# Kernel optimization log

Hardware: AMD Instinct MI355X
Metric: run time of the kernel (lower is better)

The kernel has to match this reference:

```python
import jax, jax.numpy as jnp
import numpy as np

DIM_IN = 10000
LW = [512, 512]
EW = [16, 16]


def setup_inputs() -> dict:
    key = jax.random.key(0)
    ks = jax.random.split(key, 16)
    x = jax.random.normal(ks[0], (4096, DIM_IN), dtype=jnp.float32)
    mask = jax.random.randint(ks[1], (4096, DIM_IN), 0, 2).astype(jnp.float32)
    s = 0.02
    # LNet: dim_in -> 512 -> 512 -> dim_in (tanh after hidden layers only)
    W1 = jax.random.normal(ks[2], (DIM_IN, LW[0]), dtype=jnp.float32) * s
    b1 = jnp.zeros((LW[0],), jnp.float32)
    W2 = jax.random.normal(ks[3], (LW[0], LW[1]), dtype=jnp.float32) * s
    b2 = jnp.zeros((LW[1],), jnp.float32)
    W3 = jax.random.normal(ks[4], (LW[1], DIM_IN), dtype=jnp.float32) * s
    b3 = jnp.zeros((DIM_IN,), jnp.float32)
    # ENet: 1 -> 16 -> 16 -> 1
    E1w = jax.random.normal(ks[5], (1, EW[0]), dtype=jnp.float32) * s
    E1b = jnp.zeros((EW[0],), jnp.float32)
    E2w = jax.random.normal(ks[6], (EW[0], EW[1]), dtype=jnp.float32) * s
    E2b = jnp.zeros((EW[1],), jnp.float32)
    E3w = jax.random.normal(ks[7], (EW[1], 1), dtype=jnp.float32) * s
    E3b = jnp.zeros((1,), jnp.float32)
    return {"x": x, "mask": mask, "W1": W1, "b1": b1, "W2": W2, "b2": b2,
            "W3": W3, "b3": b3, "E1w": E1w, "E1b": E1b, "E2w": E2w,
            "E2b": E2b, "E3w": E3w, "E3b": E3b}


def reference(x, mask, W1, b1, W2, b2, W3, b3, E1w, E1b, E2w, E2b, E3w, E3b):
    # LNet: two tanh hidden layers + final linear
    h = jnp.tanh(x @ W1 + b1)            # [B, 512]
    h = jnp.tanh(h @ W2 + b2)            # [B, 512]
    out = h @ W3 + b3                    # [B, dim_in]
    # ENet applied elementwise to scalar entries; original gathers x[mask>0],
    # runs ENet, adds 0.8*y residual, scatters back. Equivalent dense form:
    v = out[..., None]                   # [B, dim_in, 1]
    e = jnp.tanh(v @ E1w + E1b)          # [B, dim_in, 16]
    e = jnp.tanh(e @ E2w + E2b)          # [B, dim_in, 16]
    e = (e @ E3w + E3b)[..., 0]          # [B, dim_in]
    y = e + 0.8 * out
    return jnp.where(mask > 0, y, out)
```

## Files before the change

kernel.cpp:

```cpp
#include <hip/hip_runtime.h>
#include <stdint.h>

typedef unsigned short u16;
typedef u16 u16x8 __attribute__((ext_vector_type(8)));
typedef __bf16 bf16x8 __attribute__((ext_vector_type(8)));
typedef float f32x4 __attribute__((ext_vector_type(4)));

__device__ __forceinline__ float b2f(u16 u) {
    union { unsigned int i; float f; } c; c.i = ((unsigned int)u) << 16; return c.f;
}
__device__ __forceinline__ u16 f2b(float f) {
    unsigned int u = __float_as_uint(f);
    u += 0x7fff + ((u >> 16) & 1);
    return (u16)(u >> 16);
}

typedef const __attribute__((address_space(1))) unsigned int* gas_p;
typedef __attribute__((address_space(3))) unsigned int* las_p;
__device__ __forceinline__ void gll16(const void* g, void* l) {
    __builtin_amdgcn_global_load_lds((gas_p)g, (las_p)l, 16, 0, 0);
}

__global__ __launch_bounds__(1024) void detect_dtype(const u16* __restrict__ m,
                                                     int* __restrict__ flag) {
    __shared__ int s;
    int t = threadIdx.x;
    if (t == 0) s = 0;
    __syncthreads();
    if (m[2 * t] != 0) atomicOr(&s, 1);
    __syncthreads();
    if (t == 0) *flag = s;
}

__global__ __launch_bounds__(256) void canon_params(
        const void* b1, const void* b2, const void* b3,
        const void* E1w, const void* E1b, const void* E2w,
        const void* E2b, const void* E3w, const void* E3b,
        const int* __restrict__ flag, float* __restrict__ dst) {
    const int DT = *flag;
    int i = blockIdx.x * 256 + threadIdx.x;
    if (i >= 11345) return;
    const void* srcs[9] = {b1, b2, b3, E1w, E1b, E2w, E2b, E3w, E3b};
    const int off[10] = {0, 512, 1024, 11024, 11040, 11056, 11312, 11328, 11344, 11345};
    int s = 0;
    while (i >= off[s + 1]) ++s;
    int j = i - off[s];
    dst[i] = (DT == 1) ? b2f(((const u16*)srcs[s])[j]) : ((const float*)srcs[s])[j];
}

__global__ __launch_bounds__(256) void transpose_pad(const void* __restrict__ vin,
        u16* __restrict__ out, const int* __restrict__ flag,
        int R, int C, int ldi, int ldo) {
    const int DT = *flag;
    __shared__ __align__(16) u16 tile[64][72];
    const int rt = blockIdx.x * 64;
    const int ct = blockIdx.y * 64;
    const int t = threadIdx.x;
    const int lr = t >> 2;
    const int lc = (t & 3) * 16;
    const int r = rt + lr;
    if (r < R && (ct + lc + 15) < C) {
        if (DT == 1) {
            const u16* p = (const u16*)vin + (long)r * ldi + ct + lc;
            *(u16x8*)&tile[lr][lc]     = *(const u16x8*)p;
            *(u16x8*)&tile[lr][lc + 8] = *(const u16x8*)(p + 8);
        } else {
            const float* p = (const float*)vin + (long)r * ldi + ct + lc;
            #pragma unroll
            for (int q = 0; q < 4; ++q) {
                f32x4 v4 = *(const f32x4*)(p + q * 4);
                #pragma unroll
                for (int j = 0; j < 4; ++j) tile[lr][lc + q * 4 + j] = f2b(v4[j]);
            }
        }
    } else {
        #pragma unroll
        for (int j = 0; j < 16; ++j) {
            int c = ct + lc + j;
            u16 v = 0;
            if (r < R && c < C)
                v = (DT == 1) ? ((const u16*)vin)[(long)r * ldi + c]
                              : f2b(((const float*)vin)[(long)r * ldi + c]);
            tile[lr][lc + j] = v;
        }
    }
    __syncthreads();
    const int oc = ct + lr;
    if (oc >= C) return;
    u16x8 w0, w1;
    #pragma unroll
    for (int j = 0; j < 8; ++j) w0[j] = tile[lc + j][lr];
    #pragma unroll
    for (int j = 0; j < 8; ++j) w1[j] = tile[lc + 8 + j][lr];
    long ob = (long)oc * ldo + rt + lc;
    if (rt + lc + 15 < ldo) {
        *(u16x8*)(out + ob)     = w0;
        *(u16x8*)(out + ob + 8) = w1;
    } else {
        #pragma unroll
        for (int j = 0; j < 16; ++j) {
            int orr = rt + lc + j;
            if (orr < ldo) out[(long)oc * ldo + orr] = (j < 8) ? w0[j] : w1[j - 8];
        }
    }
}

__global__ __launch_bounds__(256) void build_elut(const float* __restrict__ P,
                                                  float* __restrict__ lut) {
    const float* E1w = P + 11024; const float* E1b = P + 11040;
    const float* E2w = P + 11056; const float* E2b = P + 11312;
    const float* E3w = P + 11328; const float* E3b = P + 11344;
    int i = blockIdx.x * 256 + threadIdx.x;
    if (i >= 4096) return;
    float v = -16.f + (float)i * (1.f / 128.f);
    float e1[16];
    #pragma unroll
    for (int j = 0; j < 16; ++j) e1[j] = tanhf(v * E1w[j] + E1b[j]);
    float e = E3b[0];
    #pragma unroll
    for (int k = 0; k < 16; ++k) {
        float s = E2b[k];
        #pragma unroll
        for (int j = 0; j < 16; ++j) s += e1[j] * E2w[j * 16 + k];
        e += tanhf(s) * E3w[k];
    }
    lut[i] = e;
}

template<int MODE, int XDT>
__global__ __launch_bounds__(256, 4) void gemm_bt(
        const void* __restrict__ A, const u16* __restrict__ Bt,
        const float* __restrict__ biasf, void* __restrict__ Cb,
        float* __restrict__ Cf, const void* __restrict__ mask,
        const float* __restrict__ lut, const int* __restrict__ flag,
        int M, int N, int K, int Kloop, int kchunk, int ldA, int ldB, int ldC) {
    if (flag && *flag != XDT) return;
    constexpr int ADT = (MODE == 2) ? XDT : 1;
    constexpr bool GLL = (ADT == 1);

    __shared__ __align__(16) u16 Alds[128 * 32];
    __shared__ __align__(16) u16 Blds[128 * 32];
    __shared__ __align__(16) float lutS[(MODE == 1) ? 4096 : 4];

    const int tid = threadIdx.x;
    const int m0 = blockIdx.x * 128;
    const int n0 = blockIdx.y * 128;
    const int lane = tid & 63;
    const int w = tid >> 6;
    const int wm = (w >> 1) * 64;
    const int wn = (w & 1) * 64;
    const int lm = lane & 15;
    const int lq = lane >> 4;

    if (MODE == 1) {
        const f32x4* s = (const f32x4*)lut;
        f32x4* d = (f32x4*)lutS;
        #pragma unroll
        for (int i = 0; i < 4; ++i) d[tid + 256 * i] = s[tid + 256 * i];
    }

    const int arow = tid >> 2;
    const int kq8 = (((tid & 3) ^ (arow & 3))) * 8;
    const long aoff = (long)(m0 + arow) * ldA + kq8;
    const long boff = (long)(n0 + arow) * ldB + kq8;
    u16* aldst0 = &Alds[tid * 8];
    u16* aldst1 = &Alds[tid * 8 + 2048];
    u16* bldst0 = &Blds[tid * 8];
    u16* bldst1 = &Blds[tid * 8 + 2048];
    const bool bv0 = (n0 + arow) < N;
    const bool bv1 = (n0 + arow + 64) < N;

    const int sx = (lq ^ (lm & 3)) * 8;
    const u16* aB = &Alds[(wm + lm) * 32 + sx];
    const u16* bB = &Blds[(wn + lm) * 32 + sx];

    const f32x4 zero = {0.f, 0.f, 0.f, 0.f};
    const u16x8 z8 = {0, 0, 0, 0, 0, 0, 0, 0};
    f32x4 acc[4][4];
    #pragma unroll
    for (int i = 0; i < 4; ++i)
        #pragma unroll
        for (int j = 0; j < 4; ++j) acc[i][j] = zero;

    int kb = 0, ke = Kloop;
    if (MODE == 2) { kb = blockIdx.z * kchunk; ke = min(Kloop, kb + kchunk); }

    const u16* Au16 = (const u16*)A;

    for (int k0 = kb; k0 < ke; k0 += 32) {
        if (GLL && (k0 + 32 <= K)) {
            __syncthreads();
            gll16(Au16 + aoff + k0, aldst0);
            gll16(Au16 + aoff + 64 * (long)ldA + k0, aldst1);
            gll16(Bt + boff + k0, bldst0);
            gll16(Bt + boff + 64 * (long)ldB + k0, bldst1);
            __syncthreads();
        } else {
            const bool av = (k0 + kq8) < K;
            u16x8 ra0 = z8, ra1 = z8;
            if (ADT == 1) {
                if (av) {
                    ra0 = *(const u16x8*)(Au16 + aoff + k0);
                    ra1 = *(const u16x8*)(Au16 + aoff + 64 * (long)ldA + k0);
                }
            } else {
                const float* Af = (const float*)A;
                if (av) {
                    f32x4 l0 = *(const f32x4*)(Af + aoff + k0);
                    f32x4 h0 = *(const f32x4*)(Af + aoff + k0 + 4);
                    f32x4 l1 = *(const f32x4*)(Af + aoff + 64 * (long)ldA + k0);
                    f32x4 h1 = *(const f32x4*)(Af + aoff + 64 * (long)ldA + k0 + 4);
                    #pragma unroll
                    for (int j = 0; j < 4; ++j) {
                        ra0[j] = f2b(l0[j]); ra0[4 + j] = f2b(h0[j]);
                        ra1[j] = f2b(l1[j]); ra1[4 + j] = f2b(h1[j]);
                    }
                }
            }
            u16x8 rb0 = bv0 ? *(const u16x8*)(Bt + boff + k0) : z8;
            u16x8 rb1 = bv1 ? *(const u16x8*)(Bt + boff + 64 * (long)ldB + k0) : z8;
            __syncthreads();
            *(u16x8*)aldst0 = ra0;
            *(u16x8*)aldst1 = ra1;
            *(u16x8*)bldst0 = rb0;
            *(u16x8*)bldst1 = rb1;
            __syncthreads();
        }
        bf16x8 a[4], b[4];
        #pragma unroll
        for (int i = 0; i < 4; ++i) a[i] = *(const bf16x8*)(aB + i * 512);
        #pragma unroll
        for (int i = 0; i < 4; ++i) b[i] = *(const bf16x8*)(bB + i * 512);
        #pragma unroll
        for (int mi = 0; mi < 4; ++mi)
            #pragma unroll
            for (int ni = 0; ni < 4; ++ni)
                acc[mi][ni] = __builtin_amdgcn_mfma_f32_16x16x32_bf16(
                    a[mi], b[ni], acc[mi][ni], 0, 0, 0);
    }

    if (MODE == 2) {
        float* dst = Cf + (long)blockIdx.z * M * (long)N;
        #pragma unroll
        for (int mi = 0; mi < 4; ++mi) {
            const int row0 = m0 + wm + mi * 16 + lq * 4;
            #pragma unroll
            for (int ni = 0; ni < 4; ++ni) {
                const int col = n0 + wn + ni * 16 + lm;
                #pragma unroll
                for (int r = 0; r < 4; ++r)
                    dst[(long)(row0 + r) * ldC + col] = acc[mi][ni][r];
            }
        }
    } else if (MODE == 0) {
        #pragma unroll
        for (int mi = 0; mi < 4; ++mi) {
            const int row0 = m0 + wm + mi * 16 + lq * 4;
            #pragma unroll
            for (int ni = 0; ni < 4; ++ni) {
                const int col = n0 + wn + ni * 16 + lm;
                const float bc = biasf[col];
                #pragma unroll
                for (int r = 0; r < 4; ++r) {
                    float v = acc[mi][ni][r] + bc;
                    ((u16*)Cb)[(long)(row0 + r) * ldC + col] = f2b(tanhf(v));
                }
            }
        }
    } else {
        #pragma unroll
        for (int mi = 0; mi < 4; ++mi) {
            const int row0 = m0 + wm + mi * 16 + lq * 4;
            #pragma unroll
            for (int ni = 0; ni < 4; ++ni) {
                const int col = n0 + wn + ni * 16 + lm;
                if (col < N) {
                    const float bc = biasf[col];
                    #pragma unroll
                    for (int r = 0; r < 4; ++r) {
                        float v = acc[mi][ni][r] + bc;
                        float fi = (v + 16.f) * 128.f + 0.5f;
                        int idx = (int)fi;
                        idx = idx < 0 ? 0 : (idx > 4095 ? 4095 : idx);
                        float y = lutS[idx] + 0.8f * v;
                        long off = (long)(row0 + r) * ldC + col;
                        float mk = (XDT == 1) ? b2f(((const u16*)mask)[off])
                                              : ((const float*)mask)[off];
                        float res = mk > 0.f ? y : v;
                        if (XDT == 1) ((u16*)Cb)[off] = f2b(res);
                        else          ((float*)Cb)[off] = res;
                    }
                }
            }
        }
    }
}

__global__ __launch_bounds__(256) void reduce_tanh8(const float* __restrict__ p,
        const float* __restrict__ biasf, u16* __restrict__ h, int MN) {
    int i = (blockIdx.x * 256 + threadIdx.x) * 4;
    if (i >= MN) return;
    f32x4 s = *(const f32x4*)(p + i);
    #pragma unroll
    for (int z = 1; z < 8; ++z) s += *(const f32x4*)(p + (long)z * MN + i);
    int col = i & 511;
    #pragma unroll
    for (int c = 0; c < 4; ++c)
        h[i + c] = f2b(tanhf(s[c] + biasf[col + c]));
}

extern "C" void kernel_launch(void* const* d_in, const int* in_sizes, int n_in,
                              void* d_out, int out_size, void* d_ws, size_t ws_size,
                              hipStream_t stream) {
    const void* x    = d_in[0];
    const void* mask = d_in[1];
    const void* W1   = d_in[2];
    const void* b1   = d_in[3];
    const void* W2   = d_in[4];
    const void* b2   = d_in[5];
    const void* W3   = d_in[6];
    const void* b3   = d_in[7];

    const int B = 4096, D = 10000, H = 512, KP = 10016;

    char* ob = (char*)d_out;
    u16*   W1T     = (u16*)ob;
    float* partial = (float*)(ob + 10256384);
    u16*   h1      = (u16*)(ob + 77365248);
    u16*   W2T     = (u16*)(ob + 10256384);

    char* ws = (char*)d_ws;
    u16*   W3T   = (u16*)ws;
    u16*   h2    = (u16*)(ws + 10240000);
    float* elut  = (float*)(ws + 14434304);
    int*   flag  = (int*)(ws + 14450688);
    float* canon = (float*)(ws + 14450704);
    float* b1f = canon, * b2f = canon + 512, * b3f = canon + 1024;

    detect_dtype<<<1, 1024, 0, stream>>>((const u16*)mask, flag);

    canon_params<<<45, 256, 0, stream>>>(b1, b2, b3, d_in[8], d_in[9],
        d_in[10], d_in[11], d_in[12], d_in[13], flag, canon);

    transpose_pad<<<dim3(157, 8), 256, 0, stream>>>(W1, W1T, flag, D, H, H, KP);
    transpose_pad<<<dim3(8, 157), 256, 0, stream>>>(W3, W3T, flag, H, D, D, H);

    build_elut<<<16, 256, 0, stream>>>(canon, elut);

    gemm_bt<2, 0><<<dim3(32, 4, 8), 256, 0, stream>>>(x, W1T, nullptr, nullptr,
        partial, nullptr, nullptr, flag, B, H, D, KP, 1280, D, KP, H);
    gemm_bt<2, 1><<<dim3(32, 4, 8), 256, 0, stream>>>(x, W1T, nullptr, nullptr,
        partial, nullptr, nullptr, flag, B, H, D, KP, 1280, D, KP, H);
    reduce_tanh8<<<(B * H) / 1024, 256, 0, stream>>>(partial, b1f, h1, B * H);

    transpose_pad<<<dim3(8, 8), 256, 0, stream>>>(W2, W2T, flag, H, H, H, H);

    gemm_bt<0, 1><<<dim3(32, 4), 256, 0, stream>>>(h1, W2T, b2f, h2, nullptr,
        nullptr, nullptr, nullptr, B, H, H, H, 0, H, H, H);

    gemm_bt<1, 0><<<dim3(32, 79), 256, 0, stream>>>(h2, W3T, b3f, d_out, nullptr,
        mask, elut, flag, B, D, H, H, 0, H, H, D);
    gemm_bt<1, 1><<<dim3(32, 79), 256, 0, stream>>>(h2, W3T, b3f, d_out, nullptr,
        mask, elut, flag, B, D, H, H, 0, H, H, D);
}
```

Measured before the change: 624.9 us.

## Fuse prep kernels, pre-convert x to bf16, drop LDS staging in GEMM

All preprocessing (dtype detection, weight transposes, bias canonicalisation, ENet LUT, and a new fp32-to-bf16 conversion of x into a padded buffer) is merged into one prep launch. The duplicate per-dtype GEMM launches are replaced by in-kernel dtype detection via a wave ballot. The GEMM no longer stages tiles through LDS and instead loads MFMA operands directly from global memory into registers. The split-K count drops from 8 to 7. The aim is fewer launches and cheaper x reads, at the cost of an extra x conversion pass and loss of LDS reuse across waves, which raises global and L2 traffic.

```diff
diff --git a/kernel.cpp b/kernel.cpp
--- a/kernel.cpp
+++ b/kernel.cpp
@@ -15,52 +15,27 @@
     return (u16)(u >> 16);
 }
 
-typedef const __attribute__((address_space(1))) unsigned int* gas_p;
-typedef __attribute__((address_space(3))) unsigned int* las_p;
-__device__ __forceinline__ void gll16(const void* g, void* l) {
-    __builtin_amdgcn_global_load_lds((gas_p)g, (las_p)l, 16, 0, 0);
-}
-
-__global__ __launch_bounds__(1024) void detect_dtype(const u16* __restrict__ m,
-                                                     int* __restrict__ flag) {
-    __shared__ int s;
-    int t = threadIdx.x;
-    if (t == 0) s = 0;
-    __syncthreads();
-    if (m[2 * t] != 0) atomicOr(&s, 1);
-    __syncthreads();
-    if (t == 0) *flag = s;
-}
-
-__global__ __launch_bounds__(256) void canon_params(
-        const void* b1, const void* b2, const void* b3,
-        const void* E1w, const void* E1b, const void* E2w,
-        const void* E2b, const void* E3w, const void* E3b,
-        const int* __restrict__ flag, float* __restrict__ dst) {
-    const int DT = *flag;
-    int i = blockIdx.x * 256 + threadIdx.x;
-    if (i >= 11345) return;
-    const void* srcs[9] = {b1, b2, b3, E1w, E1b, E2w, E2b, E3w, E3b};
-    const int off[10] = {0, 512, 1024, 11024, 11040, 11056, 11312, 11328, 11344, 11345};
-    int s = 0;
-    while (i >= off[s + 1]) ++s;
-    int j = i - off[s];
-    dst[i] = (DT == 1) ? b2f(((const u16*)srcs[s])[j]) : ((const float*)srcs[s])[j];
-}
-
-__global__ __launch_bounds__(256) void transpose_pad(const void* __restrict__ vin,
-        u16* __restrict__ out, const int* __restrict__ flag,
-        int R, int C, int ldi, int ldo) {
-    const int DT = *flag;
+__device__ __forceinline__ int detect_dt(const u16* __restrict__ m) {
+    unsigned long long b = __ballot(m[2 * (threadIdx.x & 63)] != 0);
+    return b != 0ull ? 1 : 0;
+}
+
+__device__ __forceinline__ float cv(const void* p, int j, int dt) {
+    return dt ? b2f(((const u16*)p)[j]) : ((const float*)p)[j];
+}
+
+__device__ void transpose_dev(const void* __restrict__ vin, u16* __restrict__ out,
+                              int dt, int R, int C, int ldi, int ldo,
+                              int bx, int by) {
     __shared__ __align__(16) u16 tile[64][72];
-    const int rt = blockIdx.x * 64;
-    const int ct = blockIdx.y * 64;
+    const int rt = bx * 64;
+    const int ct = by * 64;
     const int t = threadIdx.x;
     const int lr = t >> 2;
     const int lc = (t & 3) * 16;
     const int r = rt + lr;
     if (r < R && (ct + lc + 15) < C) {
-        if (DT == 1) {
+        if (dt == 1) {
             const u16* p = (const u16*)vin + (long)r * ldi + ct + lc;
             *(u16x8*)&tile[lr][lc]     = *(const u16x8*)p;
             *(u16x8*)&tile[lr][lc + 8] = *(const u16x8*)(p + 8);
@@ -79,7 +54,7 @@
             int c = ct + lc + j;
             u16 v = 0;
             if (r < R && c < C)
-                v = (DT == 1) ? ((const u16*)vin)[(long)r * ldi + c]
+                v = (dt == 1) ? ((const u16*)vin)[(long)r * ldi + c]
                               : f2b(((const float*)vin)[(long)r * ldi + c]);
             tile[lr][lc + j] = v;
         }
@@ -105,41 +80,103 @@
     }
 }
 
-__global__ __launch_bounds__(256) void build_elut(const float* __restrict__ P,
-                                                  float* __restrict__ lut) {
-    const float* E1w = P + 11024; const float* E1b = P + 11040;
-    const float* E2w = P + 11056; const float* E2b = P + 11312;
-    const float* E3w = P + 11328; const float* E3b = P + 11344;
-    int i = blockIdx.x * 256 + threadIdx.x;
-    if (i >= 4096) return;
-    float v = -16.f + (float)i * (1.f / 128.f);
-    float e1[16];
-    #pragma unroll
-    for (int j = 0; j < 16; ++j) e1[j] = tanhf(v * E1w[j] + E1b[j]);
-    float e = E3b[0];
-    #pragma unroll
-    for (int k = 0; k < 16; ++k) {
-        float s = E2b[k];
-        #pragma unroll
-        for (int j = 0; j < 16; ++j) s += e1[j] * E2w[j * 16 + k];
-        e += tanhf(s) * E3w[k];
-    }
-    lut[i] = e;
-}
-
-template<int MODE, int XDT>
+__global__ __launch_bounds__(256) void prep(
+        const void* __restrict__ x, const void* __restrict__ mask,
+        const void* __restrict__ W1, const void* __restrict__ W2,
+        const void* __restrict__ W3,
+        const void* __restrict__ b1, const void* __restrict__ b2,
+        const void* __restrict__ b3,
+        const void* __restrict__ E1w, const void* __restrict__ E1b,
+        const void* __restrict__ E2w, const void* __restrict__ E2b,
+        const void* __restrict__ E3w, const void* __restrict__ E3b,
+        u16* __restrict__ W1T, u16* __restrict__ W2T, u16* __restrict__ W3T,
+        u16* __restrict__ xb, float* __restrict__ canon,
+        float* __restrict__ elut) {
+    const int dt = detect_dt((const u16*)mask);
+    const int tid = threadIdx.x;
+    int bid = blockIdx.x;
+
+    if (bid < 1256) {
+        transpose_dev(W1, W1T, dt, 10000, 512, 512, 10016, bid >> 3, bid & 7);
+        return;
+    }
+    bid -= 1256;
+    if (bid < 1256) {
+        transpose_dev(W3, W3T, dt, 512, 10000, 10000, 512, bid & 7, bid >> 3);
+        return;
+    }
+    bid -= 1256;
+    if (bid < 64) {
+        transpose_dev(W2, W2T, dt, 512, 512, 512, 512, bid >> 3, bid & 7);
+        return;
+    }
+    bid -= 64;
+    if (bid < 44) {
+        int i = bid * 256 + tid;
+        if (i < 512)        canon[i] = cv(b1, i, dt);
+        else if (i < 1024)  canon[i] = cv(b2, i - 512, dt);
+        else if (i < 11024) canon[i] = cv(b3, i - 1024, dt);
+        return;
+    }
+    bid -= 44;
+    if (bid < 16) {
+        int i = bid * 256 + tid;
+        float v = -16.f + (float)i * (1.f / 128.f);
+        float e1[16];
+        #pragma unroll
+        for (int j = 0; j < 16; ++j)
+            e1[j] = tanhf(v * cv(E1w, j, dt) + cv(E1b, j, dt));
+        float e = cv(E3b, 0, dt);
+        #pragma unroll
+        for (int k = 0; k < 16; ++k) {
+            float s = cv(E2b, k, dt);
+            #pragma unroll
+            for (int j = 0; j < 16; ++j) s += e1[j] * cv(E2w, j * 16 + k, dt);
+            e += tanhf(s) * cv(E3w, k, dt);
+        }
+        elut[i] = e;
+        return;
+    }
+    bid -= 16;
+    if (dt != 0) return;
+    const int cb = bid % 3;
+    const int row = bid / 3;
+    const int chunk = cb * 256 + tid;
+    if (chunk >= 626) return;
+    const int col = chunk * 16;
+    u16x8 w0, w1;
+    if (col >= 10000) {
+        #pragma unroll
+        for (int j = 0; j < 8; ++j) { w0[j] = 0; w1[j] = 0; }
+    } else {
+        const float* p = (const float*)x + (long)row * 10000 + col;
+        f32x4 a = *(const f32x4*)(p);
+        f32x4 b = *(const f32x4*)(p + 4);
+        f32x4 c = *(const f32x4*)(p + 8);
+        f32x4 d = *(const f32x4*)(p + 12);
+        #pragma unroll
+        for (int j = 0; j < 4; ++j) {
+            w0[j] = f2b(a[j]); w0[4 + j] = f2b(b[j]);
+            w1[j] = f2b(c[j]); w1[4 + j] = f2b(d[j]);
+        }
+    }
+    u16* q = xb + (long)row * 10016 + col;
+    *(u16x8*)q = w0;
+    *(u16x8*)(q + 8) = w1;
+}
+
+template<int MODE>
 __global__ __launch_bounds__(256, 4) void gemm_bt(
-        const void* __restrict__ A, const u16* __restrict__ Bt,
-        const float* __restrict__ biasf, void* __restrict__ Cb,
-        float* __restrict__ Cf, const void* __restrict__ mask,
-        const float* __restrict__ lut, const int* __restrict__ flag,
-        int M, int N, int K, int Kloop, int kchunk, int ldA, int ldB, int ldC) {
-    if (flag && *flag != XDT) return;
-    constexpr int ADT = (MODE == 2) ? XDT : 1;
-    constexpr bool GLL = (ADT == 1);
-
-    __shared__ __align__(16) u16 Alds[128 * 32];
-    __shared__ __align__(16) u16 Blds[128 * 32];
+        const u16* __restrict__ A0, const u16* __restrict__ A1,
+        const u16* __restrict__ Bt, const float* __restrict__ biasf,
+        void* __restrict__ Cb, float* __restrict__ Cf,
+        const void* __restrict__ mask, const float* __restrict__ lut,
+        int M, int N, int K0, int K1, int kchunk, int ldB, int ldC) {
+    const int dt = (MODE == 0) ? 1 : detect_dt((const u16*)mask);
+    const int K = dt ? K1 : K0;
+    const u16* __restrict__ Au = dt ? A1 : A0;
+    const int ldA = K;
+
     __shared__ __align__(16) float lutS[(MODE == 1) ? 4096 : 4];
 
     const int tid = threadIdx.x;
@@ -157,22 +194,11 @@
         f32x4* d = (f32x4*)lutS;
         #pragma unroll
         for (int i = 0; i < 4; ++i) d[tid + 256 * i] = s[tid + 256 * i];
-    }
-
-    const int arow = tid >> 2;
-    const int kq8 = (((tid & 3) ^ (arow & 3))) * 8;
-    const long aoff = (long)(m0 + arow) * ldA + kq8;
-    const long boff = (long)(n0 + arow) * ldB + kq8;
-    u16* aldst0 = &Alds[tid * 8];
-    u16* aldst1 = &Alds[tid * 8 + 2048];
-    u16* bldst0 = &Blds[tid * 8];
-    u16* bldst1 = &Blds[tid * 8 + 2048];
-    const bool bv0 = (n0 + arow) < N;
-    const bool bv1 = (n0 + arow + 64) < N;
-
-    const int sx = (lq ^ (lm & 3)) * 8;
-    const u16* aB = &Alds[(wm + lm) * 32 + sx];
-    const u16* bB = &Blds[(wn + lm) * 32 + sx];
+        __syncthreads();
+    }
+
+    const long abase = (long)(m0 + wm + lm) * ldA + lq * 8;
+    const long bbase = (long)(n0 + wn + lm) * ldB + lq * 8;
 
     const f32x4 zero = {0.f, 0.f, 0.f, 0.f};
     const u16x8 z8 = {0, 0, 0, 0, 0, 0, 0, 0};
@@ -182,61 +208,44 @@
         #pragma unroll
         for (int j = 0; j < 4; ++j) acc[i][j] = zero;
 
-    int kb = 0, ke = Kloop;
-    if (MODE == 2) { kb = blockIdx.z * kchunk; ke = min(Kloop, kb + kchunk); }
-
-    const u16* Au16 = (const u16*)A;
-
-    for (int k0 = kb; k0 < ke; k0 += 32) {
-        if (GLL && (k0 + 32 <= K)) {
-            __syncthreads();
-            gll16(Au16 + aoff + k0, aldst0);
-            gll16(Au16 + aoff + 64 * (long)ldA + k0, aldst1);
-            gll16(Bt + boff + k0, bldst0);
-            gll16(Bt + boff + 64 * (long)ldB + k0, bldst1);
-            __syncthreads();
-        } else {
-            const bool av = (k0 + kq8) < K;
-            u16x8 ra0 = z8, ra1 = z8;
-            if (ADT == 1) {
-                if (av) {
-                    ra0 = *(const u16x8*)(Au16 + aoff + k0);
-                    ra1 = *(const u16x8*)(Au16 + aoff + 64 * (long)ldA + k0);
-                }
-            } else {
-                const float* Af = (const float*)A;
-                if (av) {
-                    f32x4 l0 = *(const f32x4*)(Af + aoff + k0);
-                    f32x4 h0 = *(const f32x4*)(Af + aoff + k0 + 4);
-                    f32x4 l1 = *(const f32x4*)(Af + aoff + 64 * (long)ldA + k0);
-                    f32x4 h1 = *(const f32x4*)(Af + aoff + 64 * (long)ldA + k0 + 4);
-                    #pragma unroll
-                    for (int j = 0; j < 4; ++j) {
-                        ra0[j] = f2b(l0[j]); ra0[4 + j] = f2b(h0[j]);
-                        ra1[j] = f2b(l1[j]); ra1[4 + j] = f2b(h1[j]);
-                    }
-                }
-            }
-            u16x8 rb0 = bv0 ? *(const u16x8*)(Bt + boff + k0) : z8;
-            u16x8 rb1 = bv1 ? *(const u16x8*)(Bt + boff + 64 * (long)ldB + k0) : z8;
-            __syncthreads();
-            *(u16x8*)aldst0 = ra0;
-            *(u16x8*)aldst1 = ra1;
-            *(u16x8*)bldst0 = rb0;
-            *(u16x8*)bldst1 = rb1;
-            __syncthreads();
-        }
-        bf16x8 a[4], b[4];
-        #pragma unroll
-        for (int i = 0; i < 4; ++i) a[i] = *(const bf16x8*)(aB + i * 512);
-        #pragma unroll
-        for (int i = 0; i < 4; ++i) b[i] = *(const bf16x8*)(bB + i * 512);
+    int kb = 0, ke = K;
+    if (MODE == 2) { kb = blockIdx.z * kchunk; ke = min(K, kb + kchunk); }
+    const int kfull = (ke == K) ? (K & ~31) : ke;
+
+    for (int k0 = kb; k0 < kfull; k0 += 32) {
+        u16x8 av[4], bv[4];
+        #pragma unroll
+        for (int mi = 0; mi < 4; ++mi)
+            av[mi] = *(const u16x8*)(Au + abase + (long)mi * 16 * ldA + k0);
+        #pragma unroll
+        for (int ni = 0; ni < 4; ++ni)
+            bv[ni] = *(const u16x8*)(Bt + bbase + (long)ni * 16 * ldB + k0);
         #pragma unroll
         for (int mi = 0; mi < 4; ++mi)
             #pragma unroll
             for (int ni = 0; ni < 4; ++ni)
                 acc[mi][ni] = __builtin_amdgcn_mfma_f32_16x16x32_bf16(
-                    a[mi], b[ni], acc[mi][ni], 0, 0, 0);
+                    __builtin_bit_cast(bf16x8, av[mi]),
+                    __builtin_bit_cast(bf16x8, bv[ni]), acc[mi][ni], 0, 0, 0);
+    }
+    if (kfull < ke) {
+        const int k0 = kfull;
+        const bool av_ok = (k0 + lq * 8 + 8) <= K;
+        u16x8 av[4], bv[4];
+        #pragma unroll
+        for (int mi = 0; mi < 4; ++mi)
+            av[mi] = av_ok ? *(const u16x8*)(Au + abase + (long)mi * 16 * ldA + k0)
+                           : z8;
+        #pragma unroll
+        for (int ni = 0; ni < 4; ++ni)
+            bv[ni] = *(const u16x8*)(Bt + bbase + (long)ni * 16 * ldB + k0);
+        #pragma unroll
+        for (int mi = 0; mi < 4; ++mi)
+            #pragma unroll
+            for (int ni = 0; ni < 4; ++ni)
+                acc[mi][ni] = __builtin_amdgcn_mfma_f32_16x16x32_bf16(
+                    __builtin_bit_cast(bf16x8, av[mi]),
+                    __builtin_bit_cast(bf16x8, bv[ni]), acc[mi][ni], 0, 0, 0);
     }
 
     if (MODE == 2) {
@@ -284,11 +293,11 @@
                         idx = idx < 0 ? 0 : (idx > 4095 ? 4095 : idx);
                         float y = lutS[idx] + 0.8f * v;
                         long off = (long)(row0 + r) * ldC + col;
-                        float mk = (XDT == 1) ? b2f(((const u16*)mask)[off])
-                                              : ((const float*)mask)[off];
+                        float mk = dt ? b2f(((const u16*)mask)[off])
+                                      : ((const float*)mask)[off];
                         float res = mk > 0.f ? y : v;
-                        if (XDT == 1) ((u16*)Cb)[off] = f2b(res);
-                        else          ((float*)Cb)[off] = res;
+                        if (dt) ((u16*)Cb)[off] = f2b(res);
+                        else    ((float*)Cb)[off] = res;
                     }
                 }
             }
@@ -296,13 +305,13 @@
     }
 }
 
-__global__ __launch_bounds__(256) void reduce_tanh8(const float* __restrict__ p,
+__global__ __launch_bounds__(256) void reduce_tanh7(const float* __restrict__ p,
         const float* __restrict__ biasf, u16* __restrict__ h, int MN) {
     int i = (blockIdx.x * 256 + threadIdx.x) * 4;
     if (i >= MN) return;
     f32x4 s = *(const f32x4*)(p + i);
     #pragma unroll
-    for (int z = 1; z < 8; ++z) s += *(const f32x4*)(p + (long)z * MN + i);
+    for (int z = 1; z < 7; ++z) s += *(const f32x4*)(p + (long)z * MN + i);
     int col = i & 511;
     #pragma unroll
     for (int c = 0; c < 4; ++c)
@@ -325,41 +334,30 @@
 
     char* ob = (char*)d_out;
     u16*   W1T     = (u16*)ob;
-    float* partial = (float*)(ob + 10256384);
-    u16*   h1      = (u16*)(ob + 77365248);
     u16*   W2T     = (u16*)(ob + 10256384);
+    float* partial = (float*)(ob + 10780672);
+    u16*   h1      = (u16*)(ob + 69500928);
+    u16*   xb      = (u16*)(ob + 73695232);
 
     char* ws = (char*)d_ws;
     u16*   W3T   = (u16*)ws;
     u16*   h2    = (u16*)(ws + 10240000);
     float* elut  = (float*)(ws + 14434304);
-    int*   flag  = (int*)(ws + 14450688);
-    float* canon = (float*)(ws + 14450704);
+    float* canon = (float*)(ws + 14450688);
     float* b1f = canon, * b2f = canon + 512, * b3f = canon + 1024;
 
-    detect_dtype<<<1, 1024, 0, stream>>>((const u16*)mask, flag);
-
-    canon_params<<<45, 256, 0, stream>>>(b1, b2, b3, d_in[8], d_in[9],
-        d_in[10], d_in[11], d_in[12], d_in[13], flag, canon);
-
-    transpose_pad<<<dim3(157, 8), 256, 0, stream>>>(W1, W1T, flag, D, H, H, KP);
-    transpose_pad<<<dim3(8, 157), 256, 0, stream>>>(W3, W3T, flag, H, D, D, H);
-
-    build_elut<<<16, 256, 0, stream>>>(canon, elut);
-
-    gemm_bt<2, 0><<<dim3(32, 4, 8), 256, 0, stream>>>(x, W1T, nullptr, nullptr,
-        partial, nullptr, nullptr, flag, B, H, D, KP, 1280, D, KP, H);
-    gemm_bt<2, 1><<<dim3(32, 4, 8), 256, 0, stream>>>(x, W1T, nullptr, nullptr,
-        partial, nullptr, nullptr, flag, B, H, D, KP, 1280, D, KP, H);
-    reduce_tanh8<<<(B * H) / 1024, 256, 0, stream>>>(partial, b1f, h1, B * H);
-
-    transpose_pad<<<dim3(8, 8), 256, 0, stream>>>(W2, W2T, flag, H, H, H, H);
-
-    gemm_bt<0, 1><<<dim3(32, 4), 256, 0, stream>>>(h1, W2T, b2f, h2, nullptr,
-        nullptr, nullptr, nullptr, B, H, H, H, 0, H, H, H);
-
-    gemm_bt<1, 0><<<dim3(32, 79), 256, 0, stream>>>(h2, W3T, b3f, d_out, nullptr,
-        mask, elut, flag, B, D, H, H, 0, H, H, D);
-    gemm_bt<1, 1><<<dim3(32, 79), 256, 0, stream>>>(h2, W3T, b3f, d_out, nullptr,
-        mask, elut, flag, B, D, H, H, 0, H, H, D);
-}
+    prep<<<14924, 256, 0, stream>>>(x, mask, W1, W2, W3, b1, b2, b3,
+        d_in[8], d_in[9], d_in[10], d_in[11], d_in[12], d_in[13],
+        W1T, W2T, W3T, xb, canon, elut);
+
+    gemm_bt<2><<<dim3(32, 4, 7), 256, 0, stream>>>(xb, (const u16*)x, W1T,
+        nullptr, nullptr, partial, mask, nullptr, B, H, KP, D, 1440, KP, H);
+
+    reduce_tanh7<<<(B * H) / 1024, 256, 0, stream>>>(partial, b1f, h1, B * H);
+
+    gemm_bt<0><<<dim3(32, 4), 256, 0, stream>>>(h1, h1, W2T, b2f, h2,
+        nullptr, nullptr, nullptr, B, H, H, H, 0, H, H);
+
+    gemm_bt<1><<<dim3(32, 79), 256, 0, stream>>>(h2, h2, W3T, b3f, d_out,
+        nullptr, mask, elut, B, D, H, H, 0, H, D);
+}
```

After: 854.8 us. 36.8% more time.
